# Kernel tuning notes

Hardware: AMD Instinct MI355X
Metric: run time of the kernel (lower is better)

The kernel has to match this reference:

```python
import jax, jax.numpy as jnp
import numpy as np

B, S, H = 1, 2048, 2048
QL, KVL = 1536, 512
NH, NOPE, ROPE, VD = 16, 128, 64, 128
IH, ID = 16, 128
TOPK = 512
EPS = 1e-6


def _rms_norm(x, g):
    return x * jax.lax.rsqrt(jnp.mean(x * x, -1, keepdims=True) + EPS) * g


def _layer_norm(x, g, b):
    m = jnp.mean(x, -1, keepdims=True)
    v = jnp.mean((x - m) ** 2, -1, keepdims=True)
    return (x - m) * jax.lax.rsqrt(v + EPS) * g + b


def _rope(x, cos, sin):
    # x: [B,S,h,D] (D even), cos/sin: [S,D//2]; neox-style rotate-halves
    x1, x2 = jnp.split(x, 2, -1)
    c = cos[None, :, None, :]
    s = sin[None, :, None, :]
    return jnp.concatenate([x1 * c - x2 * s, x1 * s + x2 * c], -1)


def setup_inputs() -> dict:
    key = jax.random.key(0)
    ks = jax.random.split(key, 10)
    rn = lambda k, sh: (jax.random.normal(k, sh) * 0.02).astype(jnp.float32)
    pos = jnp.arange(S, dtype=jnp.float32)
    inv = 1.0 / (10000.0 ** (jnp.arange(0, ROPE, 2, dtype=jnp.float32) / ROPE))
    ang = pos[:, None] * inv[None, :]  # [S, ROPE//2]
    return {
        "hidden_states": jax.random.normal(ks[0], (B, S, H), jnp.float32),
        "cos": jnp.cos(ang),
        "sin": jnp.sin(ang),
        "Wq_a": rn(ks[1], (H, QL)),
        "q_a_gamma": jnp.ones((QL,), jnp.float32),
        "Wq_b": rn(ks[2], (QL, NH * (NOPE + ROPE))),
        "Wkv_a": rn(ks[3], (H, KVL + ROPE)),
        "kv_a_gamma": jnp.ones((KVL,), jnp.float32),
        "Wkv_b": rn(ks[4], (KVL, NH * (NOPE + VD))),
        "Wo": rn(ks[5], (NH * VD, H)),
        "Wq_idx": rn(ks[6], (QL, IH * ID)),
        "Wk_idx": rn(ks[7], (H, ID)),
        "Ww_idx": rn(ks[8], (H, IH)),
        "kn_gamma": jnp.ones((ID,), jnp.float32),
        "kn_beta": jnp.zeros((ID,), jnp.float32),
        "topk": TOPK,
    }


def reference(hidden_states, cos, sin, Wq_a, q_a_gamma, Wq_b, Wkv_a, kv_a_gamma,
              Wkv_b, Wo, Wq_idx, Wk_idx, Ww_idx, kn_gamma, kn_beta, topk):
    b, s, _ = hidden_states.shape
    softmax_scale = (NOPE + ROPE) ** -0.5

    # ---- low-rank Q path ----
    q_a = _rms_norm(hidden_states @ Wq_a, q_a_gamma)                 # [B,S,QL]
    q = (q_a @ Wq_b).reshape(b, s, NH, NOPE + ROPE)
    q_nope, q_pe = q[..., :NOPE], _rope(q[..., NOPE:], cos, sin)

    # ---- latent KV path (MQA rope key) ----
    kv = hidden_states @ Wkv_a                                        # [B,S,KVL+ROPE]
    kv_c = _rms_norm(kv[..., :KVL], kv_a_gamma)
    k_pe = _rope(kv[..., KVL:][:, :, None, :], cos, sin)[:, :, 0]     # [B,S,ROPE]
    kvb = (kv_c @ Wkv_b).reshape(b, s, NH, NOPE + VD)
    k_nope, v = kvb[..., :NOPE], kvb[..., NOPE:]

    # ---- lightning indexer: I[t,s] = sum_h w[t,h] * relu(q_idx[t,h] . k_idx[s]) ----
    qi = (q_a @ Wq_idx).reshape(b, s, IH, ID)
    qi = jnp.concatenate([_rope(qi[..., :ROPE], cos, sin), qi[..., ROPE:]], -1)
    ki = _layer_norm(hidden_states @ Wk_idx, kn_gamma, kn_beta)       # [B,S,ID]
    ki = jnp.concatenate([_rope(ki[:, :, None, :ROPE], cos, sin)[:, :, 0], ki[..., ROPE:]], -1)
    w = hidden_states @ Ww_idx                                        # [B,S,IH]
    s_h = jax.nn.relu(jnp.einsum('bthd,bsd->bhts', qi, ki)) * (ID ** -0.5)
    idx_scores = jnp.einsum('bth,bhts->bts', w, s_h)                  # [B,S,S]

    causal = jnp.tril(jnp.ones((s, s), bool))
    idx_scores = jnp.where(causal[None], idx_scores, -jnp.inf)
    top_idx = jax.lax.top_k(idx_scores, topk)[1]                      # [B,S,topk]
    sel = jnp.zeros((b, s, s), bool).at[
        jnp.arange(b)[:, None, None], jnp.arange(s)[None, :, None], top_idx
    ].set(True)
    mask = sel & causal[None]                                         # [B,S,S]

    # ---- sparse MLA attention over selected tokens ----
    scores = (jnp.einsum('bthd,bshd->bhts', q_nope, k_nope)
              + jnp.einsum('bthd,bsd->bhts', q_pe, k_pe)) * softmax_scale
    scores = jnp.where(mask[:, None], scores, -jnp.inf)
    attn = jax.nn.softmax(scores, -1)                                 # [B,NH,S,S]
    out = jnp.einsum('bhts,bshd->bthd', attn, v).reshape(b, s, NH * VD)
    return out @ Wo                                                   # [B,S,H]
```

## Files before the change

### kernel.cpp

```cpp
#include <hip/hip_runtime.h>
#include <cstdint>
#include <cstddef>
#include <cmath>

typedef unsigned long long u64;
typedef __attribute__((ext_vector_type(8))) short bf16x8;
typedef __attribute__((ext_vector_type(4))) float f32x4;

static constexpr int S_    = 2048;
static constexpr int H_    = 2048;
static constexpr int TOPKC = 512;

#define SCALE_ATTN 0.07216878364870323f
#define ISCALE_ID  0.08838834764831845f
#define EPS_F 1e-6f

__device__ inline unsigned short f2b(float f) {
  unsigned u = __float_as_uint(f);
  return (unsigned short)((u + 0x7FFFu + ((u >> 16) & 1u)) >> 16);
}
__device__ inline float b2f(unsigned short b) {
  return __uint_as_float(((unsigned)b) << 16);
}
__device__ inline void gload16(const unsigned short* g, unsigned short* l) {
  __builtin_amdgcn_global_load_lds((const __attribute__((address_space(1))) void*)g,
                                   (__attribute__((address_space(3))) void*)l, 16, 0, 0);
}

__global__ __launch_bounds__(256) void k_gemm_bf16(
    const unsigned short* __restrict__ A, int lda,
    const unsigned short* __restrict__ Bt, int K,
    void* __restrict__ C, int ldc, int N, int out_bf16) {
  __shared__ unsigned short As[128 * 64];
  __shared__ unsigned short Bs[128 * 64];
  const int bm = blockIdx.y * 128, bn = blockIdx.x * 128;
  const int tid = threadIdx.x;
  const int lane = tid & 63, w = tid >> 6;
  const int wm = w >> 1, wn = w & 1;
  const int l15 = lane & 15, quarter = lane >> 4;
  const int srow = (lane >> 3), scol = (lane & 7) * 8;

  f32x4 acc[4][4];
#pragma unroll
  for (int i = 0; i < 4; i++)
#pragma unroll
    for (int j = 0; j < 4; j++) acc[i][j] = (f32x4){0.f, 0.f, 0.f, 0.f};

  for (int k0 = 0; k0 < K; k0 += 64) {
    __syncthreads();
#pragma unroll
    for (int i = 0; i < 4; i++) {
      int r0 = w * 32 + i * 8;
      gload16(A  + (size_t)(bm + r0 + srow) * lda + k0 + scol, &As[r0 * 64]);
      gload16(Bt + (size_t)(bn + r0 + srow) * K   + k0 + scol, &Bs[r0 * 64]);
    }
    __syncthreads();
#pragma unroll
    for (int kc = 0; kc < 2; kc++) {
      bf16x8 af[4], bfr[4];
#pragma unroll
      for (int mf = 0; mf < 4; mf++)
        af[mf] = *(const bf16x8*)(As + (wm * 64 + mf * 16 + l15) * 64 + kc * 32 + quarter * 8);
#pragma unroll
      for (int nf = 0; nf < 4; nf++)
        bfr[nf] = *(const bf16x8*)(Bs + (wn * 64 + nf * 16 + l15) * 64 + kc * 32 + quarter * 8);
#pragma unroll
      for (int mf = 0; mf < 4; mf++)
#pragma unroll
        for (int nf = 0; nf < 4; nf++)
          acc[mf][nf] = __builtin_amdgcn_mfma_f32_16x16x32_bf16(af[mf], bfr[nf], acc[mf][nf], 0, 0, 0);
    }
  }
#pragma unroll
  for (int mf = 0; mf < 4; mf++)
#pragma unroll
    for (int nf = 0; nf < 4; nf++)
#pragma unroll
      for (int r = 0; r < 4; r++) {
        int grow = bm + wm * 64 + mf * 16 + quarter * 4 + r;
        int gcol = bn + wn * 64 + nf * 16 + l15;
        if (gcol < N) {
          if (out_bf16) ((unsigned short*)C)[(size_t)grow * ldc + gcol] = f2b(acc[mf][nf][r]);
          else          ((float*)C)[(size_t)grow * ldc + gcol] = acc[mf][nf][r];
        }
      }
}

__device__ inline void tcast_tile(const float* __restrict__ W, int K, int N,
                                  unsigned short* __restrict__ dst,
                                  int r, int ntx, int tid, float (*T)[33]) {
  int xt = r % ntx, kt = r / ntx;
  int n0 = xt * 32, k0 = kt * 32;
#pragma unroll
  for (int i = 0; i < 4; i++) {
    int idx = tid + 256 * i;
    int rr = idx >> 5, c = idx & 31;
    T[rr][c] = W[(size_t)(k0 + rr) * N + n0 + c];
  }
  __syncthreads();
#pragma unroll
  for (int i = 0; i < 4; i++) {
    int idx = tid + 256 * i;
    int rr = idx >> 5, c = idx & 31;
    dst[(size_t)(n0 + rr) * K + k0 + c] = f2b(T[c][rr]);
  }
}

__global__ __launch_bounds__(256) void k_tcast_p1(
    const float* __restrict__ Wq_a, const float* __restrict__ Wkv_a,
    const float* __restrict__ Wk_idx, const float* __restrict__ Ww_idx,
    unsigned short* __restrict__ WT) {
  __shared__ float T[32][33];
  int bid = blockIdx.x, tid = threadIdx.x;
  if (bid < 3072)      tcast_tile(Wq_a,  2048, 1536, WT,                          bid,        48, tid, T);
  else if (bid < 4224) tcast_tile(Wkv_a, 2048,  576, WT + (size_t)1536 * 2048,    bid - 3072, 18, tid, T);
  else if (bid < 4480) tcast_tile(Wk_idx,2048,  128, WT + (size_t)2112 * 2048,    bid - 4224,  4, tid, T);
  else {
    int idx = (bid - 4480) * 256 + tid;
    int k = idx >> 4, n = idx & 15;
    WT[(size_t)(2240 + n) * 2048 + k] = f2b(Ww_idx[(size_t)k * 16 + n]);
  }
}

__global__ __launch_bounds__(256) void k_tcast_p2(
    const float* __restrict__ Wq_b, const float* __restrict__ Wq_idx,
    unsigned short* __restrict__ WT) {
  __shared__ float T[32][33];
  int bid = blockIdx.x, tid = threadIdx.x;
  if (bid < 4608) tcast_tile(Wq_b,   1536, 3072, WT,                        bid,        96, tid, T);
  else            tcast_tile(Wq_idx, 1536, 2048, WT + (size_t)3072 * 1536,  bid - 4608, 64, tid, T);
}

__global__ __launch_bounds__(256) void k_tcast_p3(
    const float* __restrict__ Wkv_b, const float* __restrict__ Wo,
    unsigned short* __restrict__ WT) {
  __shared__ float T[32][33];
  int bid = blockIdx.x, tid = threadIdx.x;
  if (bid < 2048) tcast_tile(Wkv_b,  512, 4096, WT,                       bid,        128, tid, T);
  else            tcast_tile(Wo,    2048, 2048, WT + (size_t)4096 * 512,  bid - 2048,  64, tid, T);
}

__global__ __launch_bounds__(256) void k_cast_bf16(const float* __restrict__ in, int pin,
                                                   unsigned short* __restrict__ outp, int pout,
                                                   int rows, int cols) {
  int cols4 = cols >> 2;
  int idx = blockIdx.x * 256 + threadIdx.x;
  if (idx >= rows * cols4) return;
  int r = idx / cols4, c = (idx - r * cols4) * 4;
  const float* ip = in + (size_t)r * pin + c;
  unsigned short* op = outp + (size_t)r * pout + c;
  op[0] = f2b(ip[0]); op[1] = f2b(ip[1]); op[2] = f2b(ip[2]); op[3] = f2b(ip[3]);
}

__global__ __launch_bounds__(256) void k_norms(
    const float* __restrict__ fat, int stride,
    const float* __restrict__ qg, const float* __restrict__ kvg,
    const float* __restrict__ kng, const float* __restrict__ knb,
    const float* __restrict__ cosb, const float* __restrict__ sinb,
    unsigned short* __restrict__ qa_b, unsigned short* __restrict__ kvc_b,
    unsigned short* __restrict__ kpe_b, unsigned short* __restrict__ ki_b) {
  int t = blockIdx.x, tid = threadIdx.x;
  const float* p = fat + (size_t)t * stride;
  __shared__ float red[256];
  __shared__ float buf[128];
  float x[6]; float s = 0.f;
#pragma unroll
  for (int i = 0; i < 6; i++) { x[i] = p[tid + 256 * i]; s += x[i] * x[i]; }
  red[tid] = s; __syncthreads();
  for (int st = 128; st > 0; st >>= 1) { if (tid < st) red[tid] += red[tid + st]; __syncthreads(); }
  float scl = rsqrtf(red[0] * (1.f / 1536.f) + EPS_F);
#pragma unroll
  for (int i = 0; i < 6; i++)
    qa_b[(size_t)t * 1536 + tid + 256 * i] = f2b(x[i] * scl * qg[tid + 256 * i]);
  __syncthreads();
  float y0 = p[1536 + tid], y1 = p[1792 + tid];
  red[tid] = y0 * y0 + y1 * y1; __syncthreads();
  for (int st = 128; st > 0; st >>= 1) { if (tid < st) red[tid] += red[tid + st]; __syncthreads(); }
  float scl2 = rsqrtf(red[0] * (1.f / 512.f) + EPS_F);
  kvc_b[(size_t)t * 512 + tid]       = f2b(y0 * scl2 * kvg[tid]);
  kvc_b[(size_t)t * 512 + 256 + tid] = f2b(y1 * scl2 * kvg[256 + tid]);
  if (tid < 32) {
    float a = p[2048 + tid], b = p[2080 + tid];
    float c = cosb[t * 32 + tid], sn = sinb[t * 32 + tid];
    kpe_b[(size_t)t * 64 + tid]      = f2b(a * c - b * sn);
    kpe_b[(size_t)t * 64 + 32 + tid] = f2b(a * sn + b * c);
  }
  __syncthreads();
  float z = (tid < 128) ? p[2112 + tid] : 0.f;
  red[tid] = z; __syncthreads();
  for (int st = 128; st > 0; st >>= 1) { if (tid < st) red[tid] += red[tid + st]; __syncthreads(); }
  float mean = red[0] * (1.f / 128.f);
  __syncthreads();
  float d = (tid < 128) ? (z - mean) : 0.f;
  red[tid] = d * d; __syncthreads();
  for (int st = 128; st > 0; st >>= 1) { if (tid < st) red[tid] += red[tid + st]; __syncthreads(); }
  float var = red[0] * (1.f / 128.f);
  if (tid < 128) buf[tid] = d * rsqrtf(var + EPS_F) * kng[tid] + knb[tid];
  __syncthreads();
  if (tid < 128) {
    float outv;
    if (tid < 32) {
      float c = cosb[t * 32 + tid], sn = sinb[t * 32 + tid];
      outv = buf[tid] * c - buf[tid + 32] * sn;
    } else if (tid < 64) {
      int j = tid - 32;
      float c = cosb[t * 32 + j], sn = sinb[t * 32 + j];
      outv = buf[j] * sn + buf[tid] * c;
    } else outv = buf[tid];
    ki_b[(size_t)t * 128 + tid] = f2b(outv);
  }
}

__global__ __launch_bounds__(256) void k_rope_b(unsigned short* __restrict__ base, int rowstride, int nh,
                                                int hstride, int off, const float* __restrict__ cosb,
                                                const float* __restrict__ sinb, int total) {
  int idx = blockIdx.x * 256 + threadIdx.x;
  if (idx >= total) return;
  int i = idx & 31, h = (idx >> 5) % nh, t = idx / (32 * nh);
  unsigned short* p = base + (size_t)t * rowstride + h * hstride + off;
  float x1 = b2f(p[i]), x2 = b2f(p[i + 32]);
  float c = cosb[t * 32 + i], s = sinb[t * 32 + i];
  p[i] = f2b(x1 * c - x2 * s);
  p[i + 32] = f2b(x1 * s + x2 * c);
}

__global__ __launch_bounds__(256) void k_idx_mfma(
    const unsigned short* __restrict__ qi_b, int qpitch,
    const unsigned short* __restrict__ ki_b,
    const float* __restrict__ wb, int wstride,
    float* __restrict__ out) {
  int bid = blockIdx.x;
  int tb = (int)((sqrtf(8.f * bid + 1.f) - 1.f) * 0.5f);
  while ((tb + 1) * (tb + 2) / 2 <= bid) tb++;
  while (tb * (tb + 1) / 2 > bid) tb--;
  int sb = bid - tb * (tb + 1) / 2;
  int t0 = tb * 64, s0 = sb * 64;

  int tid = threadIdx.x, lane = tid & 63, w = tid >> 6;
  int wm = w >> 1, wn = w & 1;
  int l15 = lane & 15, quarter = lane >> 4;

  __shared__ unsigned short Ks[64 * 128];
  __shared__ unsigned short Qs[2][64 * 128];
  __shared__ float Ws[64][16];

  int srow_[4], scc_[4];
#pragma unroll
  for (int i = 0; i < 4; i++) {
    int row = w * 16 + i * 4 + (lane >> 4);
    srow_[i] = row;
    scc_[i] = (lane & 15) ^ (row & 7);
  }
#pragma unroll
  for (int i = 0; i < 4; i++) {
    gload16(ki_b + (size_t)(s0 + srow_[i]) * 128 + scc_[i] * 8, &Ks[(w * 16 + i * 4) * 128]);
    gload16(qi_b + (size_t)(t0 + srow_[i]) * qpitch + scc_[i] * 8, &Qs[0][(w * 16 + i * 4) * 128]);
  }
  for (int i = tid; i < 64 * 16; i += 256) Ws[i >> 4][i & 15] = wb[(size_t)(t0 + (i >> 4)) * wstride + (i & 15)];
  __syncthreads();

  bf16x8 bfr[2][4];
#pragma unroll
  for (int nf = 0; nf < 2; nf++) {
    int row = wn * 32 + nf * 16 + l15;
    int rx = (row & 7) << 3;
#pragma unroll
    for (int kc = 0; kc < 4; kc++)
      bfr[nf][kc] = *(const bf16x8*)(Ks + row * 128 + ((kc * 32 + quarter * 8) ^ rx));
  }

  f32x4 acc[2][2];
#pragma unroll
  for (int mf = 0; mf < 2; mf++)
#pragma unroll
    for (int nf = 0; nf < 2; nf++) acc[mf][nf] = (f32x4){0.f, 0.f, 0.f, 0.f};

  for (int h = 0; h < 16; h++) {
    int cur = h & 1;
    if (h < 15) {
#pragma unroll
      for (int i = 0; i < 4; i++)
        gload16(qi_b + (size_t)(t0 + srow_[i]) * qpitch + (h + 1) * 128 + scc_[i] * 8,
                &Qs[cur ^ 1][(w * 16 + i * 4) * 128]);
    }
    f32x4 acch[2][2];
#pragma unroll
    for (int mf = 0; mf < 2; mf++)
#pragma unroll
      for (int nf = 0; nf < 2; nf++) acch[mf][nf] = (f32x4){0.f, 0.f, 0.f, 0.f};

    __builtin_amdgcn_s_setprio(1);
#pragma unroll
    for (int mf = 0; mf < 2; mf++) {
      int row = wm * 32 + mf * 16 + l15;
      int rx = (row & 7) << 3;
      bf16x8 af[4];
#pragma unroll
      for (int kc = 0; kc < 4; kc++)
        af[kc] = *(const bf16x8*)(Qs[cur] + row * 128 + ((kc * 32 + quarter * 8) ^ rx));
#pragma unroll
      for (int nf = 0; nf < 2; nf++)
#pragma unroll
        for (int kc = 0; kc < 4; kc++)
          acch[mf][nf] = __builtin_amdgcn_mfma_f32_16x16x32_bf16(af[kc], bfr[nf][kc], acch[mf][nf], 0, 0, 0);
    }
    __builtin_amdgcn_s_setprio(0);
#pragma unroll
    for (int mf = 0; mf < 2; mf++) {
#pragma unroll
      for (int r = 0; r < 4; r++) {
        float wv = Ws[wm * 32 + mf * 16 + quarter * 4 + r][h];
#pragma unroll
        for (int nf = 0; nf < 2; nf++)
          acc[mf][nf][r] = fmaf(wv, fmaxf(acch[mf][nf][r], 0.f), acc[mf][nf][r]);
      }
    }
    __syncthreads();
  }
#pragma unroll
  for (int mf = 0; mf < 2; mf++)
#pragma unroll
    for (int nf = 0; nf < 2; nf++)
#pragma unroll
      for (int r = 0; r < 4; r++) {
        int t = t0 + wm * 32 + mf * 16 + quarter * 4 + r;
        int s = s0 + wn * 32 + nf * 16 + l15;
        out[(size_t)t * 2048 + s] = acc[mf][nf][r] * ISCALE_ID;
      }
}

__global__ __launch_bounds__(256) void k_topk_mask(const float* __restrict__ idx_sc, u64* __restrict__ maskw) {
  int t = blockIdx.x;
  int tid = threadIdx.x;
  int n = t + 1;
  if (n <= TOPKC) {
    if (tid < 32) {
      int lo = tid * 64, hi = lo + 63;
      u64 wv;
      if (t >= hi) wv = ~0ULL;
      else if (t < lo) wv = 0ULL;
      else wv = (~0ULL) >> (63 - (t - lo));
      maskw[(size_t)t * 32 + tid] = wv;
    }
    return;
  }
  __shared__ unsigned int u[2048];
  __shared__ int hist[256];
  __shared__ int scan[256];
  __shared__ u64 mw[32];
  __shared__ int sel_b, new_target, tie_base;
  __shared__ int wcnt[4];
  if (tid < 32) mw[tid] = 0ULL;
  const float* row = idx_sc + (size_t)t * 2048;
  for (int s = tid; s < n; s += 256) {
    unsigned int bb = __float_as_uint(row[s]);
    u[s] = (bb & 0x80000000u) ? ~bb : (bb | 0x80000000u);
  }
  __syncthreads();
  unsigned int prefix = 0;
  int target = TOPKC;
  for (int shift = 24; shift >= 0; shift -= 8) {
    hist[tid] = 0;
    __syncthreads();
    unsigned int himask = (shift == 24) ? 0u : (0xFFFFFFFFu << (shift + 8));
    for (int s = tid; s < n; s += 256) {
      unsigned int uv = u[s];
      if ((uv & himask) == prefix) atomicAdd(&hist[(uv >> shift) & 0xFF], 1);
    }
    __syncthreads();
    scan[tid] = hist[tid];
    __syncthreads();
#pragma unroll
    for (int st = 1; st < 256; st <<= 1) {
      int add = (tid + st < 256) ? scan[tid + st] : 0;
      __syncthreads();
      scan[tid] += add;
      __syncthreads();
    }
    int snext = (tid == 255) ? 0 : scan[tid + 1];
    if (scan[tid] >= target && snext < target) { sel_b = tid; new_target = target - snext; }
    __syncthreads();
    prefix |= ((unsigned int)sel_b) << shift;
    target = new_target;
    __syncthreads();
  }
  if (tid == 0) tie_base = 0;
  __syncthreads();
  int wid = tid >> 6, lane = tid & 63;
  for (int s0 = 0; s0 < n; s0 += 256) {
    int s = s0 + tid;
    bool in = (s < n);
    unsigned int uv = in ? u[s] : 0u;
    bool gt = in && (uv > prefix);
    bool tie = in && (uv == prefix);
    u64 bal = __ballot(tie);
    if (lane == 0) wcnt[wid] = __popcll(bal);
    __syncthreads();
    int wbase = tie_base;
    for (int wI = 0; wI < wid; wI++) wbase += wcnt[wI];
    int rank = wbase + __popcll(bal & ((1ULL << lane) - 1ULL));
    bool sel = gt || (tie && rank < target);
    if (sel) atomicOr(&mw[s >> 6], 1ULL << (s & 63));
    __syncthreads();
    if (tid == 0) tie_base += wcnt[0] + wcnt[1] + wcnt[2] + wcnt[3];
    __syncthreads();
  }
  if (tid < 32) maskw[(size_t)t * 32 + tid] = mw[tid];
}

__global__ __launch_bounds__(256) void k_attn_mfma(
    const unsigned short* __restrict__ qb, int qpitch,
    const unsigned short* __restrict__ kvb_b,
    const unsigned short* __restrict__ kpe_b,
    const float* __restrict__ cosb, const float* __restrict__ sinb,
    const u64* __restrict__ maskw,
    unsigned short* __restrict__ attn_b,
    unsigned short* __restrict__ opart,
    float* __restrict__ mlbuf) {
  int b = blockIdx.x, h = blockIdx.y;
  int yb, k0, k1, half = 0;
  bool partial;
  if (b < 32) {
    yb = 31 - (b >> 1);
    int n = yb + 1, h1 = (n + 1) >> 1;
    half = b & 1;
    partial = true;
    k0 = half ? h1 : 0;
    k1 = half ? n : h1;
  } else {
    yb = 47 - b;
    k0 = 0; k1 = yb + 1;
    partial = false;
  }
  int t0 = yb * 64;
  int tid = threadIdx.x;
  int lane = tid & 63, wq = tid >> 6;
  int quarter = lane >> 4, l15 = lane & 15;

  __shared__ unsigned short Kd[2][64 * 192];
  __shared__ unsigned short Vts[128 * 64];

  const unsigned short* kb_base[6];
  int kb_step[6];
#pragma unroll
  for (int i = 0; i < 6; i++) {
    int slot = (wq * 6 + i) * 1024 + lane * 16;
    int rowk = slot / 384;
    int coff = slot - rowk * 384;
    int cc = (coff ^ ((rowk & 7) << 4)) >> 4;
    if (cc < 16) { kb_base[i] = kvb_b + (size_t)rowk * 4096 + h * 256 + cc * 8; kb_step[i] = 4096; }
    else         { kb_base[i] = kpe_b + (size_t)rowk * 64 + (cc - 16) * 8;      kb_step[i] = 64; }
  }
  const int vdg = tid & 15, vsp = tid >> 4;
  const unsigned short* vbase = kvb_b + (size_t)(vsp * 4) * 4096 + h * 256 + 128 + vdg * 8;

  bf16x8 qf[6];
  {
    int t = t0 + wq * 16 + l15;
    const unsigned short* qp = qb + (size_t)t * qpitch + h * 192 + quarter * 8;
#pragma unroll
    for (int kc = 0; kc < 6; kc++) qf[kc] = *(const bf16x8*)(qp + kc * 32);
    const float* cp = cosb + t * 32 + quarter * 8;
    const float* sp = sinb + t * 32 + quarter * 8;
    float4 ca = *(const float4*)cp,  cb2 = *(const float4*)(cp + 4);
    float4 sa = *(const float4*)sp,  sb2 = *(const float4*)(sp + 4);
    float carr[8] = {ca.x, ca.y, ca.z, ca.w, cb2.x, cb2.y, cb2.z, cb2.w};
    float sarr[8] = {sa.x, sa.y, sa.z, sa.w, sb2.x, sb2.y, sb2.z, sb2.w};
#pragma unroll
    for (int j = 0; j < 8; j++) {
      float x1 = b2f((unsigned short)qf[4][j]);
      float x2 = b2f((unsigned short)qf[5][j]);
      qf[4][j] = (short)f2b(x1 * carr[j] - x2 * sarr[j]);
      qf[5][j] = (short)f2b(x1 * sarr[j] + x2 * carr[j]);
    }
  }

  f32x4 o[8];
#pragma unroll
  for (int df = 0; df < 8; df++) o[df] = (f32x4){0.f, 0.f, 0.f, 0.f};
  float mcol = -__builtin_inff(), lcol = 0.f;
  const u64* mrow = maskw + (size_t)(t0 + wq * 16 + l15) * 32;

#pragma unroll
  for (int i = 0; i < 6; i++)
    gload16(kb_base[i] + (size_t)(k0 * 64) * kb_step[i], &Kd[0][(wq * 6 + i) * 512]);
  bf16x8 vr0 = *(const bf16x8*)(vbase + (size_t)(k0 * 64) * 4096);
  bf16x8 vr1 = *(const bf16x8*)(vbase + (size_t)(k0 * 64 + 1) * 4096);
  bf16x8 vr2 = *(const bf16x8*)(vbase + (size_t)(k0 * 64 + 2) * 4096);
  bf16x8 vr3 = *(const bf16x8*)(vbase + (size_t)(k0 * 64 + 3) * 4096);
  __syncthreads();
#pragma unroll
  for (int j = 0; j < 8; j++) {
    int d = vdg * 8 + j;
    uint2 w2;
    w2.x = (unsigned)(unsigned short)vr0[j] | (((unsigned)(unsigned short)vr1[j]) << 16);
    w2.y = (unsigned)(unsigned short)vr2[j] | (((unsigned)(unsigned short)vr3[j]) << 16);
    *(uint2*)((char*)Vts + d * 128 + ((vsp * 8) ^ (((d >> 2) & 7) << 4))) = w2;
  }

  int cur = 0;
  for (int k = k0; k < k1; k++, cur ^= 1) {
    __syncthreads();
    bool pf = (k + 1 < k1);
    if (pf) {
      size_t sn = (size_t)(k + 1) * 64;
#pragma unroll
      for (int i = 0; i < 6; i++)
        gload16(kb_base[i] + sn * kb_step[i], &Kd[cur ^ 1][(wq * 6 + i) * 512]);
      const unsigned short* vp = vbase + sn * 4096;
      vr0 = *(const bf16x8*)(vp);
      vr1 = *(const bf16x8*)(vp + 4096);
      vr2 = *(const bf16x8*)(vp + 8192);
      vr3 = *(const bf16x8*)(vp + 12288);
    }
    const unsigned short* Kc = Kd[cur];
    f32x4 sfT[4];
    __builtin_amdgcn_s_setprio(1);
#pragma unroll
    for (int sc = 0; sc < 4; sc++) {
      f32x4 a = (f32x4){0.f, 0.f, 0.f, 0.f};
      int row = sc * 16 + l15;
      int rx = (row & 7) << 4;
#pragma unroll
      for (int kc = 0; kc < 6; kc++) {
        int byte = row * 384 + ((kc * 64 + quarter * 16) ^ rx);
        bf16x8 kf = *(const bf16x8*)((const char*)Kc + byte);
        a = __builtin_amdgcn_mfma_f32_16x16x32_bf16(kf, qf[kc], a, 0, 0, 0);
      }
      sfT[sc] = a;
    }
    __builtin_amdgcn_s_setprio(0);
    u64 w64 = mrow[k];
    float p[4][4];
#pragma unroll
    for (int sc = 0; sc < 4; sc++)
#pragma unroll
      for (int r = 0; r < 4; r++) {
        int sbit = sc * 16 + quarter * 4 + r;
        bool sel = (w64 >> sbit) & 1ULL;
        p[sc][r] = sel ? sfT[sc][r] * SCALE_ATTN : -__builtin_inff();
      }
    float v = p[0][0];
#pragma unroll
    for (int sc = 0; sc < 4; sc++)
#pragma unroll
      for (int r = 0; r < 4; r++) v = fmaxf(v, p[sc][r]);
    v = fmaxf(v, __shfl_xor(v, 16));
    v = fmaxf(v, __shfl_xor(v, 32));
    bool need = __any(v > mcol + 8.f);
    float scl = 1.f;
    if (need) {
      float mn = fmaxf(mcol, v);
      bool dead = (mn == -__builtin_inff());
      scl = dead ? 1.f : __expf(mcol - mn);
#pragma unroll
      for (int sc = 0; sc < 4; sc++)
#pragma unroll
        for (int r = 0; r < 4; r++)
          p[sc][r] = dead ? 0.f : __expf(p[sc][r] - mn);
      mcol = dead ? mcol : mn;
    } else {
      float basem = (mcol == -__builtin_inff()) ? 0.f : mcol;
#pragma unroll
      for (int sc = 0; sc < 4; sc++)
#pragma unroll
        for (int r = 0; r < 4; r++)
          p[sc][r] = __expf(p[sc][r] - basem);
    }
    float rs = 0.f;
#pragma unroll
    for (int sc = 0; sc < 4; sc++)
#pragma unroll
      for (int r = 0; r < 4; r++) rs += p[sc][r];
    rs += __shfl_xor(rs, 16);
    rs += __shfl_xor(rs, 32);
    lcol = lcol * scl + rs;

    unsigned pk[4][2];
#pragma unroll
    for (int sc = 0; sc < 4; sc++)
#pragma unroll
      for (int rr = 0; rr < 2; rr++)
        pk[sc][rr] = (unsigned)f2b(p[sc][2 * rr]) | (((unsigned)f2b(p[sc][2 * rr + 1])) << 16);
    bf16x8 pa[2];
#pragma unroll
    for (int kc = 0; kc < 2; kc++) {
      union { unsigned d[4]; bf16x8 v; } pu;
#pragma unroll
      for (int jj = 0; jj < 4; jj++) {
        int src = ((quarter & 1) * 2 + (jj >> 1)) * 16 + l15;
        unsigned lo = (unsigned)__shfl((int)pk[kc * 2][jj & 1], src);
        unsigned hi = (unsigned)__shfl((int)pk[kc * 2 + 1][jj & 1], src);
        pu.d[jj] = (quarter < 2) ? lo : hi;
      }
      pa[kc] = pu.v;
    }
    if (need) {
      float sclr[4];
#pragma unroll
      for (int r = 0; r < 4; r++) sclr[r] = __shfl(scl, quarter * 4 + r);
#pragma unroll
      for (int df = 0; df < 8; df++)
#pragma unroll
        for (int r = 0; r < 4; r++) o[df][r] *= sclr[r];
    }
    __builtin_amdgcn_s_setprio(1);
#pragma unroll
    for (int kc = 0; kc < 2; kc++)
#pragma unroll
      for (int df = 0; df < 8; df++) {
        int d = df * 16 + l15;
        int vbyte = d * 128 + ((kc * 64 + quarter * 16) ^ (((d >> 2) & 7) << 4));
        bf16x8 vf = *(const bf16x8*)((const char*)Vts + vbyte);
        o[df] = __builtin_amdgcn_mfma_f32_16x16x32_bf16(pa[kc], vf, o[df], 0, 0, 0);
      }
    __builtin_amdgcn_s_setprio(0);
    __syncthreads();
    if (pf) {
#pragma unroll
      for (int j = 0; j < 8; j++) {
        int d = vdg * 8 + j;
        uint2 w2;
        w2.x = (unsigned)(unsigned short)vr0[j] | (((unsigned)(unsigned short)vr1[j]) << 16);
        w2.y = (unsigned)(unsigned short)vr2[j] | (((unsigned)(unsigned short)vr3[j]) << 16);
        *(uint2*)((char*)Vts + d * 128 + ((vsp * 8) ^ (((d >> 2) & 7) << 4))) = w2;
      }
    }
  }

  if (!partial) {
    float inv = (lcol > 0.f) ? 1.f / lcol : 0.f;
    float invr[4];
#pragma unroll
    for (int r = 0; r < 4; r++) invr[r] = __shfl(inv, quarter * 4 + r);
#pragma unroll
    for (int r = 0; r < 4; r++) {
      int t = t0 + wq * 16 + quarter * 4 + r;
      unsigned short* op = attn_b + (size_t)t * 2048 + h * 128 + l15;
#pragma unroll
      for (int df = 0; df < 8; df++) op[df * 16] = f2b(o[df][r] * invr[r]);
    }
  } else {
    unsigned short* ob = opart + (size_t)half * 1024 * 2048;
#pragma unroll
    for (int r = 0; r < 4; r++) {
      int t = t0 + wq * 16 + quarter * 4 + r;
      unsigned short* op = ob + (size_t)(t - 1024) * 2048 + h * 128 + l15;
#pragma unroll
      for (int df = 0; df < 8; df++) op[df * 16] = f2b(o[df][r]);
    }
    if (quarter == 0) {
      int t = t0 + wq * 16 + l15;
      float* mp = mlbuf + (((size_t)half * 1024 + (t - 1024)) * 16 + h) * 2;
      mp[0] = mcol;
      mp[1] = lcol;
    }
  }
}

__global__ __launch_bounds__(256) void k_attn_merge(
    const unsigned short* __restrict__ opart, const float* __restrict__ mlbuf,
    unsigned short* __restrict__ attn_b) {
  int idx = blockIdx.x * 256 + threadIdx.x;
  int dg = idx & 15, h = (idx >> 4) & 15, tr = idx >> 8;
  int t = 1024 + tr;
  const float* ml0 = mlbuf + ((size_t)tr * 16 + h) * 2;
  const float* ml1 = ml0 + (size_t)1024 * 16 * 2;
  float m0 = ml0[0], l0 = ml0[1];
  float m1 = ml1[0], l1 = ml1[1];
  float m = fmaxf(m0, m1);
  float w0 = (m0 == -__builtin_inff()) ? 0.f : __expf(m0 - m);
  float w1 = (m1 == -__builtin_inff()) ? 0.f : __expf(m1 - m);
  float L = l0 * w0 + l1 * w1;
  float inv = (L > 0.f) ? 1.f / L : 0.f;
  const bf16x8 o0 = *(const bf16x8*)(opart + (size_t)tr * 2048 + h * 128 + dg * 8);
  const bf16x8 o1 = *(const bf16x8*)(opart + (size_t)1024 * 2048 + (size_t)tr * 2048 + h * 128 + dg * 8);
  bf16x8 r;
#pragma unroll
  for (int j = 0; j < 8; j++) {
    float a = b2f((unsigned short)o0[j]) * w0 + b2f((unsigned short)o1[j]) * w1;
    r[j] = (short)f2b(a * inv);
  }
  *(bf16x8*)(attn_b + (size_t)t * 2048 + h * 128 + dg * 8) = r;
}

extern "C" void kernel_launch(void* const* d_in, const int* in_sizes, int n_in,
                              void* d_out, int out_size, void* d_ws, size_t ws_size,
                              hipStream_t stream) {
  const float* hs     = (const float*)d_in[0];
  const float* cosb   = (const float*)d_in[1];
  const float* sinb   = (const float*)d_in[2];
  const float* Wq_a   = (const float*)d_in[3];
  const float* q_a_g  = (const float*)d_in[4];
  const float* Wq_b   = (const float*)d_in[5];
  const float* Wkv_a  = (const float*)d_in[6];
  const float* kv_a_g = (const float*)d_in[7];
  const float* Wkv_b  = (const float*)d_in[8];
  const float* Wo     = (const float*)d_in[9];
  const float* Wq_idx = (const float*)d_in[10];
  const float* Wk_idx = (const float*)d_in[11];
  const float* Ww_idx = (const float*)d_in[12];
  const float* kn_g   = (const float*)d_in[13];
  const float* kn_b   = (const float*)d_in[14];
  float* out = (float*)d_out;

  char* base = (char*)d_ws;
  size_t off = 0;
  auto alloc = [&](size_t bytes) { void* p = base + off; off += (bytes + 255) & ~size_t(255); return p; };

  float* fat1 = (float*)alloc((size_t)S_ * 2304 * 4);
  unsigned short* attn_b = (unsigned short*)fat1;
  float* idxs = (float*)alloc((size_t)S_ * 2048 * 4);
  unsigned short* opart = (unsigned short*)idxs;
  unsigned short* fat2 = (unsigned short*)alloc((size_t)S_ * 5120 * 2);
  float* mlbuf = (float*)alloc((size_t)2 * 1024 * 16 * 2 * 4);
  u64*   maskw = (u64*)alloc((size_t)S_ * 32 * 8);
  unsigned short* hs_b  = (unsigned short*)alloc((size_t)S_ * 2048 * 2);
  unsigned short* qa_b  = (unsigned short*)alloc((size_t)S_ * 1536 * 2);
  unsigned short* kvc_b = (unsigned short*)alloc((size_t)S_ * 512 * 2);
  unsigned short* kpe_b = (unsigned short*)alloc((size_t)S_ * 64 * 2);
  unsigned short* kvb_b = (unsigned short*)alloc((size_t)S_ * 4096 * 2);
  unsigned short* ki_b  = (unsigned short*)alloc((size_t)S_ * 128 * 2);
  unsigned short* WT    = (unsigned short*)alloc((size_t)5120 * 1536 * 2);

  dim3 blk(256);

  k_cast_bf16<<<dim3((S_ * 2048 / 4) / 256), blk, 0, stream>>>(hs, 2048, hs_b, 2048, S_, 2048);
  k_tcast_p1<<<dim3(4608), blk, 0, stream>>>(Wq_a, Wkv_a, Wk_idx, Ww_idx, WT);
  k_gemm_bf16<<<dim3(18, 16), blk, 0, stream>>>(hs_b, 2048, WT, 2048, fat1, 2304, 2256, 0);
  k_norms<<<dim3(S_), blk, 0, stream>>>(fat1, 2304, q_a_g, kv_a_g, kn_g, kn_b, cosb, sinb,
                                        qa_b, kvc_b, kpe_b, ki_b);
  k_tcast_p2<<<dim3(7680), blk, 0, stream>>>(Wq_b, Wq_idx, WT);
  k_gemm_bf16<<<dim3(40, 16), blk, 0, stream>>>(qa_b, 1536, WT, 1536, fat2, 5120, 5120, 1);
  k_rope_b<<<dim3((S_ * 16 * 32) / 256), blk, 0, stream>>>(fat2 + 3072, 5120, 16, 128, 0, cosb, sinb, S_ * 16 * 32);
  k_tcast_p3<<<dim3(6144), blk, 0, stream>>>(Wkv_b, Wo, WT);
  k_gemm_bf16<<<dim3(32, 16), blk, 0, stream>>>(kvc_b, 512, WT, 512, kvb_b, 4096, 4096, 1);
  k_idx_mfma<<<dim3(528), blk, 0, stream>>>(fat2 + 3072, 5120, ki_b, fat1 + 2240, 2304, idxs);
  k_topk_mask<<<dim3(S_), blk, 0, stream>>>(idxs, maskw);
  k_attn_mfma<<<dim3(48, 16), blk, 0, stream>>>(fat2, 5120, kvb_b, kpe_b, cosb, sinb, maskw,
                                                attn_b, opart, mlbuf);
  k_attn_merge<<<dim3((1024 * 16 * 16) / 256), blk, 0, stream>>>(opart, mlbuf, attn_b);
  k_gemm_bf16<<<dim3(16, 16), blk, 0, stream>>>(attn_b, 2048, WT + (size_t)4096 * 512, 2048, out, 2048, 2048, 0);

  (void)in_sizes; (void)n_in; (void)out_size; (void)ws_size;
}
```

Before: 370.7 us.

## Drop attention split-K merge, swizzle GEMM tiles per XCD, fuse hidden cast

The attention kernel no longer splits long causal row blocks into two partial halves followed by a merge kernel. Instead each (row block, head) workgroup processes its whole key range, and the row-block order is reversed for half the heads to balance load. The GEMM remaps workgroup IDs so consecutive tiles land on the same XCD for better L2 locality. The hidden-state bf16 cast is folded into the first transpose-cast kernel, saving one launch. Removing the split trades the merge kernel and partial buffers for a longer critical path on the last row blocks, since there are now only 512 attention workgroups.

```diff
diff --git a/kernel.cpp b/kernel.cpp
--- a/kernel.cpp
+++ b/kernel.cpp
@@ -33,7 +33,13 @@
     void* __restrict__ C, int ldc, int N, int out_bf16) {
   __shared__ unsigned short As[128 * 64];
   __shared__ unsigned short Bs[128 * 64];
-  const int bm = blockIdx.y * 128, bn = blockIdx.x * 128;
+  int nwg = gridDim.x * gridDim.y;
+  int orig = blockIdx.y * gridDim.x + blockIdx.x;
+  int q = nwg >> 3, r = nwg & 7;
+  int xcd = orig & 7, sub = orig >> 3;
+  int wgid = (xcd < r ? xcd * (q + 1) : r * (q + 1) + (xcd - r) * q) + sub;
+  int by = wgid / gridDim.x, bx = wgid - by * gridDim.x;
+  const int bm = by * 128, bn = bx * 128;
   const int tid = threadIdx.x;
   const int lane = tid & 63, w = tid >> 6;
   const int wm = w >> 1, wn = w & 1;
@@ -76,12 +82,12 @@
 #pragma unroll
     for (int nf = 0; nf < 4; nf++)
 #pragma unroll
-      for (int r = 0; r < 4; r++) {
-        int grow = bm + wm * 64 + mf * 16 + quarter * 4 + r;
+      for (int r2 = 0; r2 < 4; r2++) {
+        int grow = bm + wm * 64 + mf * 16 + quarter * 4 + r2;
         int gcol = bn + wn * 64 + nf * 16 + l15;
         if (gcol < N) {
-          if (out_bf16) ((unsigned short*)C)[(size_t)grow * ldc + gcol] = f2b(acc[mf][nf][r]);
-          else          ((float*)C)[(size_t)grow * ldc + gcol] = acc[mf][nf][r];
+          if (out_bf16) ((unsigned short*)C)[(size_t)grow * ldc + gcol] = f2b(acc[mf][nf][r2]);
+          else          ((float*)C)[(size_t)grow * ldc + gcol] = acc[mf][nf][r2];
         }
       }
 }
@@ -109,16 +115,22 @@
 __global__ __launch_bounds__(256) void k_tcast_p1(
     const float* __restrict__ Wq_a, const float* __restrict__ Wkv_a,
     const float* __restrict__ Wk_idx, const float* __restrict__ Ww_idx,
+    const float* __restrict__ hs, unsigned short* __restrict__ hs_b,
     unsigned short* __restrict__ WT) {
   __shared__ float T[32][33];
   int bid = blockIdx.x, tid = threadIdx.x;
   if (bid < 3072)      tcast_tile(Wq_a,  2048, 1536, WT,                          bid,        48, tid, T);
   else if (bid < 4224) tcast_tile(Wkv_a, 2048,  576, WT + (size_t)1536 * 2048,    bid - 3072, 18, tid, T);
   else if (bid < 4480) tcast_tile(Wk_idx,2048,  128, WT + (size_t)2112 * 2048,    bid - 4224,  4, tid, T);
-  else {
+  else if (bid < 4608) {
     int idx = (bid - 4480) * 256 + tid;
     int k = idx >> 4, n = idx & 15;
     WT[(size_t)(2240 + n) * 2048 + k] = f2b(Ww_idx[(size_t)k * 16 + n]);
+  } else {
+    int idx = ((bid - 4608) * 256 + tid) * 4;
+    const float* ip = hs + idx;
+    unsigned short* op = hs_b + idx;
+    op[0] = f2b(ip[0]); op[1] = f2b(ip[1]); op[2] = f2b(ip[2]); op[3] = f2b(ip[3]);
   }
 }
 
@@ -138,18 +150,6 @@
   int bid = blockIdx.x, tid = threadIdx.x;
   if (bid < 2048) tcast_tile(Wkv_b,  512, 4096, WT,                       bid,        128, tid, T);
   else            tcast_tile(Wo,    2048, 2048, WT + (size_t)4096 * 512,  bid - 2048,  64, tid, T);
-}
-
-__global__ __launch_bounds__(256) void k_cast_bf16(const float* __restrict__ in, int pin,
-                                                   unsigned short* __restrict__ outp, int pout,
-                                                   int rows, int cols) {
-  int cols4 = cols >> 2;
-  int idx = blockIdx.x * 256 + threadIdx.x;
-  if (idx >= rows * cols4) return;
-  int r = idx / cols4, c = (idx - r * cols4) * 4;
-  const float* ip = in + (size_t)r * pin + c;
-  unsigned short* op = outp + (size_t)r * pout + c;
-  op[0] = f2b(ip[0]); op[1] = f2b(ip[1]); op[2] = f2b(ip[2]); op[3] = f2b(ip[3]);
 }
 
 __global__ __launch_bounds__(256) void k_norms(
@@ -414,24 +414,10 @@
     const unsigned short* __restrict__ kpe_b,
     const float* __restrict__ cosb, const float* __restrict__ sinb,
     const u64* __restrict__ maskw,
-    unsigned short* __restrict__ attn_b,
-    unsigned short* __restrict__ opart,
-    float* __restrict__ mlbuf) {
-  int b = blockIdx.x, h = blockIdx.y;
-  int yb, k0, k1, half = 0;
-  bool partial;
-  if (b < 32) {
-    yb = 31 - (b >> 1);
-    int n = yb + 1, h1 = (n + 1) >> 1;
-    half = b & 1;
-    partial = true;
-    k0 = half ? h1 : 0;
-    k1 = half ? n : h1;
-  } else {
-    yb = 47 - b;
-    k0 = 0; k1 = yb + 1;
-    partial = false;
-  }
+    unsigned short* __restrict__ attn_b) {
+  int ybm = blockIdx.x;
+  int h = blockIdx.y;
+  int yb = (h < 8) ? ybm : (31 - ybm);
   int t0 = yb * 64;
   int tid = threadIdx.x;
   int lane = tid & 63, wq = tid >> 6;
@@ -480,14 +466,14 @@
   for (int df = 0; df < 8; df++) o[df] = (f32x4){0.f, 0.f, 0.f, 0.f};
   float mcol = -__builtin_inff(), lcol = 0.f;
   const u64* mrow = maskw + (size_t)(t0 + wq * 16 + l15) * 32;
-
-#pragma unroll
-  for (int i = 0; i < 6; i++)
-    gload16(kb_base[i] + (size_t)(k0 * 64) * kb_step[i], &Kd[0][(wq * 6 + i) * 512]);
-  bf16x8 vr0 = *(const bf16x8*)(vbase + (size_t)(k0 * 64) * 4096);
-  bf16x8 vr1 = *(const bf16x8*)(vbase + (size_t)(k0 * 64 + 1) * 4096);
-  bf16x8 vr2 = *(const bf16x8*)(vbase + (size_t)(k0 * 64 + 2) * 4096);
-  bf16x8 vr3 = *(const bf16x8*)(vbase + (size_t)(k0 * 64 + 3) * 4096);
+  int nsb = yb + 1;
+
+#pragma unroll
+  for (int i = 0; i < 6; i++) gload16(kb_base[i], &Kd[0][(wq * 6 + i) * 512]);
+  bf16x8 vr0 = *(const bf16x8*)(vbase);
+  bf16x8 vr1 = *(const bf16x8*)(vbase + 4096);
+  bf16x8 vr2 = *(const bf16x8*)(vbase + 8192);
+  bf16x8 vr3 = *(const bf16x8*)(vbase + 12288);
   __syncthreads();
 #pragma unroll
   for (int j = 0; j < 8; j++) {
@@ -499,11 +485,11 @@
   }
 
   int cur = 0;
-  for (int k = k0; k < k1; k++, cur ^= 1) {
-    __syncthreads();
-    bool pf = (k + 1 < k1);
+  for (int sb = 0; sb < nsb; sb++, cur ^= 1) {
+    __syncthreads();
+    bool pf = (sb + 1 < nsb);
     if (pf) {
-      size_t sn = (size_t)(k + 1) * 64;
+      size_t sn = (size_t)(sb + 1) * 64;
 #pragma unroll
       for (int i = 0; i < 6; i++)
         gload16(kb_base[i] + sn * kb_step[i], &Kd[cur ^ 1][(wq * 6 + i) * 512]);
@@ -530,7 +516,7 @@
       sfT[sc] = a;
     }
     __builtin_amdgcn_s_setprio(0);
-    u64 w64 = mrow[k];
+    u64 w64 = mrow[sb];
     float p[4][4];
 #pragma unroll
     for (int sc = 0; sc < 4; sc++)
@@ -627,61 +613,17 @@
       }
     }
   }
-
-  if (!partial) {
-    float inv = (lcol > 0.f) ? 1.f / lcol : 0.f;
-    float invr[4];
-#pragma unroll
-    for (int r = 0; r < 4; r++) invr[r] = __shfl(inv, quarter * 4 + r);
-#pragma unroll
-    for (int r = 0; r < 4; r++) {
-      int t = t0 + wq * 16 + quarter * 4 + r;
-      unsigned short* op = attn_b + (size_t)t * 2048 + h * 128 + l15;
-#pragma unroll
-      for (int df = 0; df < 8; df++) op[df * 16] = f2b(o[df][r] * invr[r]);
-    }
-  } else {
-    unsigned short* ob = opart + (size_t)half * 1024 * 2048;
-#pragma unroll
-    for (int r = 0; r < 4; r++) {
-      int t = t0 + wq * 16 + quarter * 4 + r;
-      unsigned short* op = ob + (size_t)(t - 1024) * 2048 + h * 128 + l15;
-#pragma unroll
-      for (int df = 0; df < 8; df++) op[df * 16] = f2b(o[df][r]);
-    }
-    if (quarter == 0) {
-      int t = t0 + wq * 16 + l15;
-      float* mp = mlbuf + (((size_t)half * 1024 + (t - 1024)) * 16 + h) * 2;
-      mp[0] = mcol;
-      mp[1] = lcol;
-    }
-  }
-}
-
-__global__ __launch_bounds__(256) void k_attn_merge(
-    const unsigned short* __restrict__ opart, const float* __restrict__ mlbuf,
-    unsigned short* __restrict__ attn_b) {
-  int idx = blockIdx.x * 256 + threadIdx.x;
-  int dg = idx & 15, h = (idx >> 4) & 15, tr = idx >> 8;
-  int t = 1024 + tr;
-  const float* ml0 = mlbuf + ((size_t)tr * 16 + h) * 2;
-  const float* ml1 = ml0 + (size_t)1024 * 16 * 2;
-  float m0 = ml0[0], l0 = ml0[1];
-  float m1 = ml1[0], l1 = ml1[1];
-  float m = fmaxf(m0, m1);
-  float w0 = (m0 == -__builtin_inff()) ? 0.f : __expf(m0 - m);
-  float w1 = (m1 == -__builtin_inff()) ? 0.f : __expf(m1 - m);
-  float L = l0 * w0 + l1 * w1;
-  float inv = (L > 0.f) ? 1.f / L : 0.f;
-  const bf16x8 o0 = *(const bf16x8*)(opart + (size_t)tr * 2048 + h * 128 + dg * 8);
-  const bf16x8 o1 = *(const bf16x8*)(opart + (size_t)1024 * 2048 + (size_t)tr * 2048 + h * 128 + dg * 8);
-  bf16x8 r;
-#pragma unroll
-  for (int j = 0; j < 8; j++) {
-    float a = b2f((unsigned short)o0[j]) * w0 + b2f((unsigned short)o1[j]) * w1;
-    r[j] = (short)f2b(a * inv);
-  }
-  *(bf16x8*)(attn_b + (size_t)t * 2048 + h * 128 + dg * 8) = r;
+  float inv = (lcol > 0.f) ? 1.f / lcol : 0.f;
+  float invr[4];
+#pragma unroll
+  for (int r = 0; r < 4; r++) invr[r] = __shfl(inv, quarter * 4 + r);
+#pragma unroll
+  for (int r = 0; r < 4; r++) {
+    int t = t0 + wq * 16 + quarter * 4 + r;
+    unsigned short* op = attn_b + (size_t)t * 2048 + h * 128 + l15;
+#pragma unroll
+    for (int df = 0; df < 8; df++) op[df * 16] = f2b(o[df][r] * invr[r]);
+  }
 }
 
 extern "C" void kernel_launch(void* const* d_in, const int* in_sizes, int n_in,
@@ -711,9 +653,7 @@
   float* fat1 = (float*)alloc((size_t)S_ * 2304 * 4);
   unsigned short* attn_b = (unsigned short*)fat1;
   float* idxs = (float*)alloc((size_t)S_ * 2048 * 4);
-  unsigned short* opart = (unsigned short*)idxs;
   unsigned short* fat2 = (unsigned short*)alloc((size_t)S_ * 5120 * 2);
-  float* mlbuf = (float*)alloc((size_t)2 * 1024 * 16 * 2 * 4);
   u64*   maskw = (u64*)alloc((size_t)S_ * 32 * 8);
   unsigned short* hs_b  = (unsigned short*)alloc((size_t)S_ * 2048 * 2);
   unsigned short* qa_b  = (unsigned short*)alloc((size_t)S_ * 1536 * 2);
@@ -725,8 +665,7 @@
 
   dim3 blk(256);
 
-  k_cast_bf16<<<dim3((S_ * 2048 / 4) / 256), blk, 0, stream>>>(hs, 2048, hs_b, 2048, S_, 2048);
-  k_tcast_p1<<<dim3(4608), blk, 0, stream>>>(Wq_a, Wkv_a, Wk_idx, Ww_idx, WT);
+  k_tcast_p1<<<dim3(8704), blk, 0, stream>>>(Wq_a, Wkv_a, Wk_idx, Ww_idx, hs, hs_b, WT);
   k_gemm_bf16<<<dim3(18, 16), blk, 0, stream>>>(hs_b, 2048, WT, 2048, fat1, 2304, 2256, 0);
   k_norms<<<dim3(S_), blk, 0, stream>>>(fat1, 2304, q_a_g, kv_a_g, kn_g, kn_b, cosb, sinb,
                                         qa_b, kvc_b, kpe_b, ki_b);
@@ -737,9 +676,7 @@
   k_gemm_bf16<<<dim3(32, 16), blk, 0, stream>>>(kvc_b, 512, WT, 512, kvb_b, 4096, 4096, 1);
   k_idx_mfma<<<dim3(528), blk, 0, stream>>>(fat2 + 3072, 5120, ki_b, fat1 + 2240, 2304, idxs);
   k_topk_mask<<<dim3(S_), blk, 0, stream>>>(idxs, maskw);
-  k_attn_mfma<<<dim3(48, 16), blk, 0, stream>>>(fat2, 5120, kvb_b, kpe_b, cosb, sinb, maskw,
-                                                attn_b, opart, mlbuf);
-  k_attn_merge<<<dim3((1024 * 16 * 16) / 256), blk, 0, stream>>>(opart, mlbuf, attn_b);
+  k_attn_mfma<<<dim3(32, 16), blk, 0, stream>>>(fat2, 5120, kvb_b, kpe_b, cosb, sinb, maskw, attn_b);
   k_gemm_bf16<<<dim3(16, 16), blk, 0, stream>>>(attn_b, 2048, WT + (size_t)4096 * 512, 2048, out, 2048, 2048, 0);
 
   (void)in_sizes; (void)n_in; (void)out_size; (void)ws_size;
```

Measured after the change: 420.6 us. 13.5% more time.
